# Performance work log

Hardware: AMD Instinct MI355X
Metric: run time of the kernel (lower is better)

The kernel has to match this reference:

```python
import jax, jax.numpy as jnp
import numpy as np

B, S, D, H, DFF = 4, 2048, 1024, 16, 4096
HD = D // H
EPS = 1e-12

def _layernorm(x, g, b):
    mu = jnp.mean(x, axis=-1, keepdims=True)
    var = jnp.mean(jnp.square(x - mu), axis=-1, keepdims=True)
    return (x - mu) * jax.lax.rsqrt(var + EPS) * g + b

def setup_inputs() -> dict:
    key = jax.random.key(0)
    ks = jax.random.split(key, 12)
    sd = 0.02
    inp = {
        'hidden_states': jax.random.normal(ks[0], (B, S, D), jnp.float32),
        'attention_mask': jnp.zeros((B, 1, 1, S), jnp.float32),
        'Wq': jax.random.normal(ks[1], (D, D), jnp.float32) * sd,
        'bq': jnp.zeros((D,), jnp.float32),
        'Wk': jax.random.normal(ks[2], (D, D), jnp.float32) * sd,
        'bk': jnp.zeros((D,), jnp.float32),
        'Wv': jax.random.normal(ks[3], (D, D), jnp.float32) * sd,
        'bv': jnp.zeros((D,), jnp.float32),
        'Wo': jax.random.normal(ks[4], (D, D), jnp.float32) * sd,
        'bo': jnp.zeros((D,), jnp.float32),
        'ln1_g': jnp.ones((D,), jnp.float32),
        'ln1_b': jnp.zeros((D,), jnp.float32),
        'Wi': jax.random.normal(ks[5], (D, DFF), jnp.float32) * sd,
        'bi': jnp.zeros((DFF,), jnp.float32),
        'Wo2': jax.random.normal(ks[6], (DFF, D), jnp.float32) * sd,
        'bo2': jnp.zeros((D,), jnp.float32),
        'ln2_g': jnp.ones((D,), jnp.float32),
        'ln2_b': jnp.zeros((D,), jnp.float32),
    }
    return inp

def reference(hidden_states, attention_mask, Wq, bq, Wk, bk, Wv, bv, Wo, bo,
              ln1_g, ln1_b, Wi, bi, Wo2, bo2, ln2_g, ln2_b):
    x = hidden_states  # [B,S,D]
    # project and split heads -> [B,H,S,hd]
    def heads(t):
        return t.reshape(B, S, H, HD).transpose(0, 2, 1, 3)
    q = heads(x @ Wq + bq)
    k = heads(x @ Wk + bk)
    v = heads(x @ Wv + bv)
    scores = jnp.einsum('bhqd,bhkd->bhqk', q, k) / np.float32(np.sqrt(HD))
    scores = scores + attention_mask  # additive mask broadcast [B,1,1,S]
    weights = jax.nn.softmax(scores, axis=-1)
    ctx = jnp.einsum('bhqk,bhkd->bhqd', weights, v)
    ctx = ctx.transpose(0, 2, 1, 3).reshape(B, S, D)
    attn_out = _layernorm(ctx @ Wo + bo + x, ln1_g, ln1_b)
    # FFN (gelu) with residual + LayerNorm
    h = jax.nn.gelu(attn_out @ Wi + bi, approximate=False)
    out = _layernorm(h @ Wo2 + bo2 + attn_out, ln2_g, ln2_b)
    return out
```

## Files before the change

### kernel.cpp

```cpp
#include <hip/hip_runtime.h>
#include <hip/hip_bf16.h>
#include <math.h>

#define B_   4
#define S_   2048
#define D_   1024
#define H_   16
#define HD_  64
#define DFF_ 4096
#define M_   (B_*S_)

typedef __bf16 bf16x8 __attribute__((ext_vector_type(8)));
typedef __bf16 bf16x4 __attribute__((ext_vector_type(4)));
typedef float  floatx4 __attribute__((ext_vector_type(4)));

__device__ __forceinline__ float  b2f(__bf16 v) { return (float)v; }
__device__ __forceinline__ __bf16 f2b(float v)  { return (__bf16)v; }

__device__ __forceinline__ void async_ld16(const void* g, void* l) {
    __builtin_amdgcn_global_load_lds(
        (const __attribute__((address_space(1))) unsigned int*)g,
        (__attribute__((address_space(3))) unsigned int*)l, 16, 0, 0);
}

__global__ void transpose_conv_kernel(const float* __restrict__ in,
                                      __bf16* __restrict__ out, int R, int C,
                                      float scale)
{
    __shared__ float t[32][33];
    int c0 = blockIdx.x * 32, r0 = blockIdx.y * 32;
    int tx = threadIdx.x, ty = threadIdx.y;
    for (int i = ty; i < 32; i += 8)
        t[i][tx] = in[(long)(r0 + i) * C + c0 + tx];
    __syncthreads();
    for (int i = ty; i < 32; i += 8)
        out[(long)(c0 + i) * R + r0 + tx] = f2b(t[tx][i] * scale);
}

__global__ void vt_transpose_kernel(const __bf16* __restrict__ qkv,
                                    __bf16* __restrict__ vtg)
{
    __shared__ __bf16 t[32][34];
    int b  = blockIdx.z;
    int h  = blockIdx.y >> 1;
    int d0 = (blockIdx.y & 1) * 32;
    int s0 = blockIdx.x * 32;
    int tx = threadIdx.x, ty = threadIdx.y;
    for (int i = ty; i < 32; i += 8)
        t[i][tx] = qkv[(long)(b * S_ + s0 + i) * 3072 + 2048 + h * 64 + d0 + tx];
    __syncthreads();
    for (int i = ty; i < 32; i += 8)
        vtg[((long)(b * H_ + h) * 64 + d0 + i) * S_ + s0 + tx] = t[tx][i];
}

__global__ void f2b_kernel(const float* __restrict__ in, __bf16* __restrict__ out,
                           long n)
{
    long i = ((long)blockIdx.x * 256 + threadIdx.x) * 8;
    if (i >= n) return;
    float4 a = *(const float4*)&in[i];
    float4 c = *(const float4*)&in[i + 4];
    union { __bf16 h[8]; uint4 u; } p;
    p.h[0] = f2b(a.x); p.h[1] = f2b(a.y); p.h[2] = f2b(a.z); p.h[3] = f2b(a.w);
    p.h[4] = f2b(c.x); p.h[5] = f2b(c.y); p.h[6] = f2b(c.z); p.h[7] = f2b(c.w);
    *(uint4*)&out[i] = p.u;
}

__global__ void bias_concat_kernel(const float* __restrict__ bq,
                                   const float* __restrict__ bk,
                                   const float* __restrict__ bv,
                                   float* __restrict__ dst)
{
    int i = blockIdx.x * 256 + threadIdx.x;
    if (i >= 3 * D_) return;
    float v = (i < D_) ? bq[i] * 0.125f
            : (i < 2 * D_) ? bk[i - D_] : bv[i - 2 * D_];
    dst[i] = v;
}

template<int MODE>
__global__ __launch_bounds__(256, 2)
void gemm_kernel(const __bf16* __restrict__ A, const __bf16* __restrict__ Bt,
                 const float* __restrict__ bias, const float* __restrict__ resid,
                 float* __restrict__ Cf, __bf16* __restrict__ Cb,
                 int M, int N, int K)
{
    __shared__ __bf16 sA[128 * 64];
    __shared__ __bf16 sB[128 * 64];

    const int tid  = threadIdx.x;
    const int lane = tid & 63;
    const int wave = tid >> 6;
    const int wm   = (wave >> 1) * 64;
    const int wn   = (wave & 1) * 64;
    const long bm  = (long)blockIdx.y * 128;
    const long bn  = (long)blockIdx.x * 128;

    floatx4 acc[4][4];
#pragma unroll
    for (int i = 0; i < 4; ++i)
#pragma unroll
        for (int j = 0; j < 4; ++j)
#pragma unroll
            for (int r = 0; r < 4; ++r) acc[i][j][r] = 0.0f;

    const int mrow = lane & 15;
    const int quad = lane >> 4;
    const int koff0 = ((0 * 4 + quad) ^ (mrow & 7)) * 8;
    const int koff1 = ((1 * 4 + quad) ^ (mrow & 7)) * 8;

    for (int k0 = 0; k0 < K; k0 += 64) {
        __syncthreads();
#pragma unroll
        for (int t = 0; t < 4; ++t) {
            int ci  = tid + t * 256;
            int row = ci >> 3;
            int col = ((ci & 7) ^ (row & 7)) << 3;
            async_ld16(A  + (bm + row) * (long)K + k0 + col, &sA[ci * 8]);
            async_ld16(Bt + (bn + row) * (long)K + k0 + col, &sB[ci * 8]);
        }
        __syncthreads();

#pragma unroll
        for (int s = 0; s < 2; ++s) {
            const int ko = s ? koff1 : koff0;
            bf16x8 a[4], b[4];
#pragma unroll
            for (int i = 0; i < 4; ++i)
                a[i] = *(const bf16x8*)&sA[(wm + i * 16 + mrow) * 64 + ko];
#pragma unroll
            for (int j = 0; j < 4; ++j)
                b[j] = *(const bf16x8*)&sB[(wn + j * 16 + mrow) * 64 + ko];
#pragma unroll
            for (int i = 0; i < 4; ++i)
#pragma unroll
                for (int j = 0; j < 4; ++j)
                    acc[i][j] = __builtin_amdgcn_mfma_f32_16x16x32_bf16(
                        a[i], b[j], acc[i][j], 0, 0, 0);
        }
    }

    const int rq = quad * 4;
    const int cn = lane & 15;
#pragma unroll
    for (int i = 0; i < 4; ++i) {
#pragma unroll
        for (int j = 0; j < 4; ++j) {
            long col = bn + wn + j * 16 + cn;
            float bv = bias[col];
#pragma unroll
            for (int r = 0; r < 4; ++r) {
                long row = bm + wm + i * 16 + rq + r;
                float v = acc[i][j][r] + bv;
                if (MODE == 0) {
                    Cb[row * N + col] = f2b(v);
                } else if (MODE == 1) {
                    Cf[row * N + col] = v + resid[row * N + col];
                } else {
                    float g = 0.5f * v * (1.0f + erff(v * 0.70710678118654752f));
                    Cb[row * N + col] = f2b(g);
                }
            }
        }
    }
}

__global__ __launch_bounds__(256, 2)
void attn_kernel(const __bf16* __restrict__ QKV, const __bf16* __restrict__ VT,
                 const float* __restrict__ mask, __bf16* __restrict__ ctx)
{
    __shared__ __bf16 Qs[64 * 64];
    __shared__ __bf16 Ks[64 * 64];
    __shared__ __bf16 Vt[64 * 64];
    __shared__ __bf16 Ps[64 * 64];

    const int tid  = threadIdx.x;
    const int lane = tid & 63;
    const int wave = tid >> 6;
    const int w16  = wave * 16;
    const int b    = blockIdx.z, h = blockIdx.y;
    const int q0   = blockIdx.x * 64;
    const int cn   = lane & 15;
    const int quad = lane >> 4;
    const int rq   = quad * 4;
    const int koff0 = ((0 * 4 + quad) ^ (cn & 7)) * 8;
    const int koff1 = ((1 * 4 + quad) ^ (cn & 7)) * 8;

#pragma unroll
    for (int t = 0; t < 2; ++t) {
        int ci = tid + t * 256;
        int qr = ci >> 3, dc = ((ci & 7) ^ (qr & 7)) << 3;
        async_ld16(QKV + (long)(b * S_ + q0 + qr) * 3072 + h * 64 + dc,
                   &Qs[ci * 8]);
    }
    __syncthreads();
    const bf16x8 aq0 = *(const bf16x8*)&Qs[(w16 + cn) * 64 + koff0];
    const bf16x8 aq1 = *(const bf16x8*)&Qs[(w16 + cn) * 64 + koff1];

    float l_[4];
    floatx4 o_[4];
#pragma unroll
    for (int r = 0; r < 4; ++r) l_[r] = 0.0f;
#pragma unroll
    for (int jt = 0; jt < 4; ++jt)
#pragma unroll
        for (int r = 0; r < 4; ++r) o_[jt][r] = 0.0f;

    const long vbase = ((long)(b * H_ + h) * 64) * S_;

    for (int k0 = 0; k0 < S_; k0 += 64) {
        __syncthreads();
#pragma unroll
        for (int t = 0; t < 2; ++t) {
            int ci = tid + t * 256;
            int kr = ci >> 3, dc = ((ci & 7) ^ (kr & 7)) << 3;
            async_ld16(QKV + (long)(b * S_ + k0 + kr) * 3072 + 1024 + h * 64 + dc,
                       &Ks[ci * 8]);
            int vd = ci >> 3, kc = ((ci & 7) ^ (vd & 7)) << 3;
            async_ld16(VT + vbase + (long)vd * S_ + k0 + kc, &Vt[ci * 8]);
        }
        __syncthreads();

        floatx4 st[4];
#pragma unroll
        for (int jt = 0; jt < 4; ++jt)
#pragma unroll
            for (int r = 0; r < 4; ++r) st[jt][r] = 0.0f;
#pragma unroll
        for (int jt = 0; jt < 4; ++jt) {
            bf16x8 b0 = *(const bf16x8*)&Ks[(jt * 16 + cn) * 64 + koff0];
            bf16x8 b1 = *(const bf16x8*)&Ks[(jt * 16 + cn) * 64 + koff1];
            st[jt] = __builtin_amdgcn_mfma_f32_16x16x32_bf16(aq0, b0, st[jt], 0, 0, 0);
            st[jt] = __builtin_amdgcn_mfma_f32_16x16x32_bf16(aq1, b1, st[jt], 0, 0, 0);
        }
#pragma unroll
        for (int jt = 0; jt < 4; ++jt) {
            float mv = mask[(long)b * S_ + k0 + jt * 16 + cn] - 8.0f;
#pragma unroll
            for (int r = 0; r < 4; ++r) {
                float p = __expf(st[jt][r] + mv);
                st[jt][r] = p;
                l_[r] += p;
            }
        }
#pragma unroll
        for (int jt = 0; jt < 4; ++jt)
#pragma unroll
            for (int r = 0; r < 4; ++r) {
                int prow = w16 + rq + r;
                int pcol = (((jt * 2 + (cn >> 3)) ^ (prow & 7)) << 3) + (cn & 7);
                Ps[prow * 64 + pcol] = f2b(st[jt][r]);
            }

        {
            bf16x8 ap0 = *(const bf16x8*)&Ps[(w16 + cn) * 64 + koff0];
            bf16x8 ap1 = *(const bf16x8*)&Ps[(w16 + cn) * 64 + koff1];
#pragma unroll
            for (int jt = 0; jt < 4; ++jt) {
                bf16x8 b0 = *(const bf16x8*)&Vt[(jt * 16 + cn) * 64 + koff0];
                bf16x8 b1 = *(const bf16x8*)&Vt[(jt * 16 + cn) * 64 + koff1];
                o_[jt] = __builtin_amdgcn_mfma_f32_16x16x32_bf16(ap0, b0, o_[jt], 0, 0, 0);
                o_[jt] = __builtin_amdgcn_mfma_f32_16x16x32_bf16(ap1, b1, o_[jt], 0, 0, 0);
            }
        }
    }

#pragma unroll
    for (int r = 0; r < 4; ++r) {
        float l = l_[r];
        l += __shfl_xor(l, 1);
        l += __shfl_xor(l, 2);
        l += __shfl_xor(l, 4);
        l += __shfl_xor(l, 8);
        float linv = 1.0f / l;
        long rowg = (long)(b * S_ + q0 + w16 + rq + r) * D_ + h * 64;
#pragma unroll
        for (int jt = 0; jt < 4; ++jt)
            ctx[rowg + jt * 16 + cn] = f2b(o_[jt][r] * linv);
    }
}

__global__ __launch_bounds__(256)
void ln_kernel(const float* __restrict__ X, const float* __restrict__ gamma,
               const float* __restrict__ beta, float* __restrict__ out,
               __bf16* __restrict__ outb)
{
    const long row = blockIdx.x;
    const int tid = threadIdx.x;
    const float* x = X + row * D_;
    float4 v = *(const float4*)&x[tid * 4];
    float s  = v.x + v.y + v.z + v.w;
    float s2 = v.x * v.x + v.y * v.y + v.z * v.z + v.w * v.w;
    for (int off = 32; off > 0; off >>= 1) {
        s  += __shfl_down(s, off);
        s2 += __shfl_down(s2, off);
    }
    __shared__ float red[8];
    int wave = tid >> 6, lane = tid & 63;
    if (lane == 0) { red[wave] = s; red[4 + wave] = s2; }
    __syncthreads();
    float ts  = red[0] + red[1] + red[2] + red[3];
    float ts2 = red[4] + red[5] + red[6] + red[7];
    float mu  = ts * (1.0f / D_);
    float var = ts2 * (1.0f / D_) - mu * mu;
    float rs  = rsqrtf(fmaxf(var, 0.0f) + 1e-12f);
    float4 g = *(const float4*)&gamma[tid * 4];
    float4 b = *(const float4*)&beta[tid * 4];
    float4 o;
    o.x = (v.x - mu) * rs * g.x + b.x;
    o.y = (v.y - mu) * rs * g.y + b.y;
    o.z = (v.z - mu) * rs * g.z + b.z;
    o.w = (v.w - mu) * rs * g.w + b.w;
    *(float4*)&out[row * D_ + tid * 4] = o;
    if (outb) {
        bf16x4 ob;
        ob[0] = f2b(o.x); ob[1] = f2b(o.y); ob[2] = f2b(o.z); ob[3] = f2b(o.w);
        *(bf16x4*)&outb[row * D_ + tid * 4] = ob;
    }
}

extern "C" void kernel_launch(void* const* d_in, const int* in_sizes, int n_in,
                              void* d_out, int out_size, void* d_ws, size_t ws_size,
                              hipStream_t stream)
{
    const float* hid  = (const float*)d_in[0];
    const float* mask = (const float*)d_in[1];
    const float* Wq   = (const float*)d_in[2];
    const float* bq   = (const float*)d_in[3];
    const float* Wk   = (const float*)d_in[4];
    const float* bk   = (const float*)d_in[5];
    const float* Wv   = (const float*)d_in[6];
    const float* bv   = (const float*)d_in[7];
    const float* Wo   = (const float*)d_in[8];
    const float* bo   = (const float*)d_in[9];
    const float* g1   = (const float*)d_in[10];
    const float* b1   = (const float*)d_in[11];
    const float* Wi   = (const float*)d_in[12];
    const float* bi   = (const float*)d_in[13];
    const float* Wo2  = (const float*)d_in[14];
    const float* bo2  = (const float*)d_in[15];
    const float* g2   = (const float*)d_in[16];
    const float* b2   = (const float*)d_in[17];
    float* out = (float*)d_out;

    char* w = (char*)d_ws;
    auto take = [&](size_t bytes) { char* p = w; w += bytes; return p; };
    __bf16* wqkvb = (__bf16*)take((size_t)3 * D_ * D_ * 2);
    __bf16* wob   = (__bf16*)take((size_t)D_ * D_ * 2);
    __bf16* wib   = (__bf16*)take((size_t)D_ * DFF_ * 2);
    __bf16* wo2b  = (__bf16*)take((size_t)D_ * DFF_ * 2);
    float*  qkvbias = (float*)take(16384);
    __bf16* qkv   = (__bf16*)take((size_t)M_ * 3 * D_ * 2);
    __bf16* ctxb  = (__bf16*)take((size_t)M_ * D_ * 2);
    __bf16* hb    = (__bf16*)take((size_t)M_ * D_ * 2);
    float*  tmp      = (float*)take((size_t)M_ * D_ * 4);
    float*  attn_out = (float*)take((size_t)M_ * D_ * 4);
    __bf16* hbuf = qkv;
    __bf16* vtg  = hb;
    __bf16* attn_out_b = hb;
    (void)in_sizes; (void)n_in; (void)out_size; (void)ws_size;

    dim3 tb(32, 8);
    transpose_conv_kernel<<<dim3(D_/32, D_/32), tb, 0, stream>>>(Wq, wqkvb,            D_, D_, 0.125f);
    transpose_conv_kernel<<<dim3(D_/32, D_/32), tb, 0, stream>>>(Wk, wqkvb + D_*D_,    D_, D_, 1.0f);
    transpose_conv_kernel<<<dim3(D_/32, D_/32), tb, 0, stream>>>(Wv, wqkvb + 2*D_*D_,  D_, D_, 1.0f);
    transpose_conv_kernel<<<dim3(D_/32, D_/32), tb, 0, stream>>>(Wo, wob, D_, D_, 1.0f);
    transpose_conv_kernel<<<dim3(DFF_/32, D_/32), tb, 0, stream>>>(Wi, wib, D_, DFF_, 1.0f);
    transpose_conv_kernel<<<dim3(D_/32, DFF_/32), tb, 0, stream>>>(Wo2, wo2b, DFF_, D_, 1.0f);
    bias_concat_kernel<<<12, 256, 0, stream>>>(bq, bk, bv, qkvbias);
    f2b_kernel<<<(M_*D_/8 + 255)/256, 256, 0, stream>>>(hid, hb, (long)M_*D_);

    gemm_kernel<0><<<dim3(3*D_/128, M_/128), 256, 0, stream>>>(
        hb, wqkvb, qkvbias, nullptr, nullptr, qkv, M_, 3*D_, D_);

    vt_transpose_kernel<<<dim3(S_/32, H_*2, B_), tb, 0, stream>>>(qkv, vtg);

    attn_kernel<<<dim3(S_/64, H_, B_), 256, 0, stream>>>(qkv, vtg, mask, ctxb);

    gemm_kernel<1><<<dim3(D_/128, M_/128), 256, 0, stream>>>(
        ctxb, wob, bo, hid, tmp, nullptr, M_, D_, D_);
    ln_kernel<<<M_, 256, 0, stream>>>(tmp, g1, b1, attn_out, attn_out_b);

    gemm_kernel<2><<<dim3(DFF_/128, M_/128), 256, 0, stream>>>(
        attn_out_b, wib, bi, nullptr, nullptr, hbuf, M_, DFF_, D_);
    gemm_kernel<1><<<dim3(D_/128, M_/128), 256, 0, stream>>>(
        hbuf, wo2b, bo2, attn_out, tmp, nullptr, M_, D_, DFF_);
    ln_kernel<<<M_, 256, 0, stream>>>(tmp, g2, b2, out, nullptr);
}
```

Baseline: 581.5 us.

## Switch attention to 32x32x16 MFMA with 128-query tiles per block

The attention kernel now processes 128 query rows per block (32 per wave) and uses 32x32x16 bf16 MFMA instructions instead of 16x16x32. Each K/V tile loaded into shared memory is reused across twice as many queries, halving K/V global traffic and the number of blocks. The row-sum reduction gains an extra shuffle step and register pressure per wave rises (two 16-wide accumulators plus 16 row sums), which may lower occupancy.

```diff
diff --git a/kernel.cpp b/kernel.cpp
--- a/kernel.cpp
+++ b/kernel.cpp
@@ -13,6 +13,7 @@
 typedef __bf16 bf16x8 __attribute__((ext_vector_type(8)));
 typedef __bf16 bf16x4 __attribute__((ext_vector_type(4)));
 typedef float  floatx4 __attribute__((ext_vector_type(4)));
+typedef float  floatx16 __attribute__((ext_vector_type(16)));
 
 __device__ __forceinline__ float  b2f(__bf16 v) { return (float)v; }
 __device__ __forceinline__ __bf16 f2b(float v)  { return (__bf16)v; }
@@ -169,42 +170,42 @@
 void attn_kernel(const __bf16* __restrict__ QKV, const __bf16* __restrict__ VT,
                  const float* __restrict__ mask, __bf16* __restrict__ ctx)
 {
-    __shared__ __bf16 Qs[64 * 64];
+    __shared__ __bf16 Qs[128 * 64];
     __shared__ __bf16 Ks[64 * 64];
     __shared__ __bf16 Vt[64 * 64];
-    __shared__ __bf16 Ps[64 * 64];
+    __shared__ __bf16 Ps[128 * 64];
 
     const int tid  = threadIdx.x;
     const int lane = tid & 63;
     const int wave = tid >> 6;
-    const int w16  = wave * 16;
+    const int w32  = wave * 32;
     const int b    = blockIdx.z, h = blockIdx.y;
-    const int q0   = blockIdx.x * 64;
-    const int cn   = lane & 15;
-    const int quad = lane >> 4;
-    const int rq   = quad * 4;
-    const int koff0 = ((0 * 4 + quad) ^ (cn & 7)) * 8;
-    const int koff1 = ((1 * 4 + quad) ^ (cn & 7)) * 8;
-
-#pragma unroll
-    for (int t = 0; t < 2; ++t) {
+    const int q0   = blockIdx.x * 128;
+    const int l31  = lane & 31;
+    const int half = lane >> 5;
+
+    int koff[4];
+#pragma unroll
+    for (int s = 0; s < 4; ++s)
+        koff[s] = ((s * 2 + half) ^ (l31 & 7)) * 8;
+
+#pragma unroll
+    for (int t = 0; t < 4; ++t) {
         int ci = tid + t * 256;
         int qr = ci >> 3, dc = ((ci & 7) ^ (qr & 7)) << 3;
         async_ld16(QKV + (long)(b * S_ + q0 + qr) * 3072 + h * 64 + dc,
                    &Qs[ci * 8]);
     }
     __syncthreads();
-    const bf16x8 aq0 = *(const bf16x8*)&Qs[(w16 + cn) * 64 + koff0];
-    const bf16x8 aq1 = *(const bf16x8*)&Qs[(w16 + cn) * 64 + koff1];
-
-    float l_[4];
-    floatx4 o_[4];
-#pragma unroll
-    for (int r = 0; r < 4; ++r) l_[r] = 0.0f;
-#pragma unroll
-    for (int jt = 0; jt < 4; ++jt)
-#pragma unroll
-        for (int r = 0; r < 4; ++r) o_[jt][r] = 0.0f;
+    bf16x8 aq[4];
+#pragma unroll
+    for (int s = 0; s < 4; ++s)
+        aq[s] = *(const bf16x8*)&Qs[(w32 + l31) * 64 + koff[s]];
+
+    float l_[16];
+    floatx16 o_[2];
+#pragma unroll
+    for (int r = 0; r < 16; ++r) { l_[r] = 0.0f; o_[0][r] = 0.0f; o_[1][r] = 0.0f; }
 
     const long vbase = ((long)(b * H_ + h) * 64) * S_;
 
@@ -216,67 +217,65 @@
             int kr = ci >> 3, dc = ((ci & 7) ^ (kr & 7)) << 3;
             async_ld16(QKV + (long)(b * S_ + k0 + kr) * 3072 + 1024 + h * 64 + dc,
                        &Ks[ci * 8]);
-            int vd = ci >> 3, kc = ((ci & 7) ^ (vd & 7)) << 3;
-            async_ld16(VT + vbase + (long)vd * S_ + k0 + kc, &Vt[ci * 8]);
+            async_ld16(VT + vbase + (long)kr * S_ + k0 + dc, &Vt[ci * 8]);
         }
         __syncthreads();
 
-        floatx4 st[4];
-#pragma unroll
-        for (int jt = 0; jt < 4; ++jt)
-#pragma unroll
-            for (int r = 0; r < 4; ++r) st[jt][r] = 0.0f;
-#pragma unroll
-        for (int jt = 0; jt < 4; ++jt) {
-            bf16x8 b0 = *(const bf16x8*)&Ks[(jt * 16 + cn) * 64 + koff0];
-            bf16x8 b1 = *(const bf16x8*)&Ks[(jt * 16 + cn) * 64 + koff1];
-            st[jt] = __builtin_amdgcn_mfma_f32_16x16x32_bf16(aq0, b0, st[jt], 0, 0, 0);
-            st[jt] = __builtin_amdgcn_mfma_f32_16x16x32_bf16(aq1, b1, st[jt], 0, 0, 0);
-        }
-#pragma unroll
-        for (int jt = 0; jt < 4; ++jt) {
-            float mv = mask[(long)b * S_ + k0 + jt * 16 + cn] - 8.0f;
-#pragma unroll
-            for (int r = 0; r < 4; ++r) {
-                float p = __expf(st[jt][r] + mv);
-                st[jt][r] = p;
+        floatx16 st[2];
+#pragma unroll
+        for (int r = 0; r < 16; ++r) { st[0][r] = 0.0f; st[1][r] = 0.0f; }
+#pragma unroll
+        for (int nt = 0; nt < 2; ++nt) {
+#pragma unroll
+            for (int s = 0; s < 4; ++s) {
+                bf16x8 bk = *(const bf16x8*)&Ks[(nt * 32 + l31) * 64 + koff[s]];
+                st[nt] = __builtin_amdgcn_mfma_f32_32x32x16_bf16(aq[s], bk, st[nt], 0, 0, 0);
+            }
+        }
+#pragma unroll
+        for (int nt = 0; nt < 2; ++nt) {
+            float mv = mask[(long)b * S_ + k0 + nt * 32 + l31] - 8.0f;
+#pragma unroll
+            for (int r = 0; r < 16; ++r) {
+                float p = __expf(st[nt][r] + mv);
+                st[nt][r] = p;
                 l_[r] += p;
             }
         }
 #pragma unroll
-        for (int jt = 0; jt < 4; ++jt)
-#pragma unroll
-            for (int r = 0; r < 4; ++r) {
-                int prow = w16 + rq + r;
-                int pcol = (((jt * 2 + (cn >> 3)) ^ (prow & 7)) << 3) + (cn & 7);
-                Ps[prow * 64 + pcol] = f2b(st[jt][r]);
-            }
-
-        {
-            bf16x8 ap0 = *(const bf16x8*)&Ps[(w16 + cn) * 64 + koff0];
-            bf16x8 ap1 = *(const bf16x8*)&Ps[(w16 + cn) * 64 + koff1];
-#pragma unroll
-            for (int jt = 0; jt < 4; ++jt) {
-                bf16x8 b0 = *(const bf16x8*)&Vt[(jt * 16 + cn) * 64 + koff0];
-                bf16x8 b1 = *(const bf16x8*)&Vt[(jt * 16 + cn) * 64 + koff1];
-                o_[jt] = __builtin_amdgcn_mfma_f32_16x16x32_bf16(ap0, b0, o_[jt], 0, 0, 0);
-                o_[jt] = __builtin_amdgcn_mfma_f32_16x16x32_bf16(ap1, b1, o_[jt], 0, 0, 0);
-            }
-        }
-    }
-
-#pragma unroll
-    for (int r = 0; r < 4; ++r) {
+        for (int nt = 0; nt < 2; ++nt)
+#pragma unroll
+            for (int r = 0; r < 16; ++r) {
+                int prow = w32 + (r & 3) + 8 * (r >> 2) + 4 * half;
+                int col  = nt * 32 + l31;
+                int sc   = (((col >> 3) ^ (prow & 7)) << 3) | (col & 7);
+                Ps[prow * 64 + sc] = f2b(st[nt][r]);
+            }
+
+#pragma unroll
+        for (int s = 0; s < 4; ++s) {
+            bf16x8 ap = *(const bf16x8*)&Ps[(w32 + l31) * 64 + koff[s]];
+#pragma unroll
+            for (int nt = 0; nt < 2; ++nt) {
+                bf16x8 bv = *(const bf16x8*)&Vt[(nt * 32 + l31) * 64 + koff[s]];
+                o_[nt] = __builtin_amdgcn_mfma_f32_32x32x16_bf16(ap, bv, o_[nt], 0, 0, 0);
+            }
+        }
+    }
+
+#pragma unroll
+    for (int r = 0; r < 16; ++r) {
         float l = l_[r];
         l += __shfl_xor(l, 1);
         l += __shfl_xor(l, 2);
         l += __shfl_xor(l, 4);
         l += __shfl_xor(l, 8);
+        l += __shfl_xor(l, 16);
         float linv = 1.0f / l;
-        long rowg = (long)(b * S_ + q0 + w16 + rq + r) * D_ + h * 64;
-#pragma unroll
-        for (int jt = 0; jt < 4; ++jt)
-            ctx[rowg + jt * 16 + cn] = f2b(o_[jt][r] * linv);
+        int row = w32 + (r & 3) + 8 * (r >> 2) + 4 * half;
+        long rowg = (long)(b * S_ + q0 + row) * D_ + h * 64;
+        ctx[rowg + l31]      = f2b(o_[0][r] * linv);
+        ctx[rowg + 32 + l31] = f2b(o_[1][r] * linv);
     }
 }
 
@@ -375,7 +374,7 @@
 
     vt_transpose_kernel<<<dim3(S_/32, H_*2, B_), tb, 0, stream>>>(qkv, vtg);
 
-    attn_kernel<<<dim3(S_/64, H_, B_), 256, 0, stream>>>(qkv, vtg, mask, ctxb);
+    attn_kernel<<<dim3(S_/128, H_, B_), 256, 0, stream>>>(qkv, vtg, mask, ctxb);
 
     gemm_kernel<1><<<dim3(D_/128, M_/128), 256, 0, stream>>>(
         ctxb, wob, bo, hid, tmp, nullptr, M_, D_, D_);
```

After: 622.9 us. 1.07x slower.

## Double attention query tile per block and fold log2e into Q scaling

Applied to the files above, without the earlier changes.

The attention kernel now handles 128 query rows per block, 32 per wave, so each K and V tile loaded into shared memory feeds twice as many MFMAs. This halves the K/V traffic per query. The Q and P buffers are merged to hold shared-memory use roughly constant. The softmax scale now includes log2(e) through the Q weights and bias so the kernel can call exp2f instead of __expf. The trade-off is more accumulator registers per thread and half as many blocks, which lowers parallelism.

```diff
diff --git a/kernel.cpp b/kernel.cpp
--- a/kernel.cpp
+++ b/kernel.cpp
@@ -69,11 +69,11 @@
 __global__ void bias_concat_kernel(const float* __restrict__ bq,
                                    const float* __restrict__ bk,
                                    const float* __restrict__ bv,
-                                   float* __restrict__ dst)
+                                   float* __restrict__ dst, float qscale)
 {
     int i = blockIdx.x * 256 + threadIdx.x;
     if (i >= 3 * D_) return;
-    float v = (i < D_) ? bq[i] * 0.125f
+    float v = (i < D_) ? bq[i] * qscale
             : (i < 2 * D_) ? bk[i - D_] : bv[i - 2 * D_];
     dst[i] = v;
 }
@@ -169,17 +169,16 @@
 void attn_kernel(const __bf16* __restrict__ QKV, const __bf16* __restrict__ VT,
                  const float* __restrict__ mask, __bf16* __restrict__ ctx)
 {
-    __shared__ __bf16 Qs[64 * 64];
+    __shared__ __bf16 QPs[128 * 64];
     __shared__ __bf16 Ks[64 * 64];
     __shared__ __bf16 Vt[64 * 64];
-    __shared__ __bf16 Ps[64 * 64];
 
     const int tid  = threadIdx.x;
     const int lane = tid & 63;
     const int wave = tid >> 6;
-    const int w16  = wave * 16;
+    const int w32  = wave * 32;
     const int b    = blockIdx.z, h = blockIdx.y;
-    const int q0   = blockIdx.x * 64;
+    const int q0   = blockIdx.x * 128;
     const int cn   = lane & 15;
     const int quad = lane >> 4;
     const int rq   = quad * 4;
@@ -187,26 +186,33 @@
     const int koff1 = ((1 * 4 + quad) ^ (cn & 7)) * 8;
 
 #pragma unroll
-    for (int t = 0; t < 2; ++t) {
+    for (int t = 0; t < 4; ++t) {
         int ci = tid + t * 256;
         int qr = ci >> 3, dc = ((ci & 7) ^ (qr & 7)) << 3;
         async_ld16(QKV + (long)(b * S_ + q0 + qr) * 3072 + h * 64 + dc,
-                   &Qs[ci * 8]);
+                   &QPs[ci * 8]);
     }
     __syncthreads();
-    const bf16x8 aq0 = *(const bf16x8*)&Qs[(w16 + cn) * 64 + koff0];
-    const bf16x8 aq1 = *(const bf16x8*)&Qs[(w16 + cn) * 64 + koff1];
-
-    float l_[4];
-    floatx4 o_[4];
-#pragma unroll
-    for (int r = 0; r < 4; ++r) l_[r] = 0.0f;
-#pragma unroll
-    for (int jt = 0; jt < 4; ++jt)
-#pragma unroll
-        for (int r = 0; r < 4; ++r) o_[jt][r] = 0.0f;
+    bf16x8 aq[2][2];
+#pragma unroll
+    for (int g = 0; g < 2; ++g) {
+        aq[g][0] = *(const bf16x8*)&QPs[(w32 + g * 16 + cn) * 64 + koff0];
+        aq[g][1] = *(const bf16x8*)&QPs[(w32 + g * 16 + cn) * 64 + koff1];
+    }
+
+    float l_[2][4];
+    floatx4 o_[2][4];
+#pragma unroll
+    for (int g = 0; g < 2; ++g)
+#pragma unroll
+        for (int r = 0; r < 4; ++r) {
+            l_[g][r] = 0.0f;
+#pragma unroll
+            for (int jt = 0; jt < 4; ++jt) o_[g][jt][r] = 0.0f;
+        }
 
     const long vbase = ((long)(b * H_ + h) * 64) * S_;
+    const float LOG2E = 1.44269504088896f;
 
     for (int k0 = 0; k0 < S_; k0 += 64) {
         __syncthreads();
@@ -216,68 +222,79 @@
             int kr = ci >> 3, dc = ((ci & 7) ^ (kr & 7)) << 3;
             async_ld16(QKV + (long)(b * S_ + k0 + kr) * 3072 + 1024 + h * 64 + dc,
                        &Ks[ci * 8]);
-            int vd = ci >> 3, kc = ((ci & 7) ^ (vd & 7)) << 3;
-            async_ld16(VT + vbase + (long)vd * S_ + k0 + kc, &Vt[ci * 8]);
+            async_ld16(VT + vbase + (long)kr * S_ + k0 + dc, &Vt[ci * 8]);
         }
         __syncthreads();
 
-        floatx4 st[4];
-#pragma unroll
-        for (int jt = 0; jt < 4; ++jt)
-#pragma unroll
-            for (int r = 0; r < 4; ++r) st[jt][r] = 0.0f;
+        floatx4 st[2][4];
+#pragma unroll
+        for (int g = 0; g < 2; ++g)
+#pragma unroll
+            for (int jt = 0; jt < 4; ++jt)
+#pragma unroll
+                for (int r = 0; r < 4; ++r) st[g][jt][r] = 0.0f;
+#pragma unroll
+        for (int s = 0; s < 2; ++s) {
+            const int ko = s ? koff1 : koff0;
+#pragma unroll
+            for (int jt = 0; jt < 4; ++jt) {
+                bf16x8 bk = *(const bf16x8*)&Ks[(jt * 16 + cn) * 64 + ko];
+                st[0][jt] = __builtin_amdgcn_mfma_f32_16x16x32_bf16(aq[0][s], bk, st[0][jt], 0, 0, 0);
+                st[1][jt] = __builtin_amdgcn_mfma_f32_16x16x32_bf16(aq[1][s], bk, st[1][jt], 0, 0, 0);
+            }
+        }
 #pragma unroll
         for (int jt = 0; jt < 4; ++jt) {
-            bf16x8 b0 = *(const bf16x8*)&Ks[(jt * 16 + cn) * 64 + koff0];
-            bf16x8 b1 = *(const bf16x8*)&Ks[(jt * 16 + cn) * 64 + koff1];
-            st[jt] = __builtin_amdgcn_mfma_f32_16x16x32_bf16(aq0, b0, st[jt], 0, 0, 0);
-            st[jt] = __builtin_amdgcn_mfma_f32_16x16x32_bf16(aq1, b1, st[jt], 0, 0, 0);
-        }
-#pragma unroll
-        for (int jt = 0; jt < 4; ++jt) {
-            float mv = mask[(long)b * S_ + k0 + jt * 16 + cn] - 8.0f;
-#pragma unroll
-            for (int r = 0; r < 4; ++r) {
-                float p = __expf(st[jt][r] + mv);
-                st[jt][r] = p;
-                l_[r] += p;
+            float mv = (mask[(long)b * S_ + k0 + jt * 16 + cn] - 8.0f) * LOG2E;
+#pragma unroll
+            for (int g = 0; g < 2; ++g)
+#pragma unroll
+                for (int r = 0; r < 4; ++r) {
+                    float p = exp2f(st[g][jt][r] + mv);
+                    st[g][jt][r] = p;
+                    l_[g][r] += p;
+                }
+        }
+#pragma unroll
+        for (int g = 0; g < 2; ++g)
+#pragma unroll
+            for (int jt = 0; jt < 4; ++jt)
+#pragma unroll
+                for (int r = 0; r < 4; ++r) {
+                    int prow = w32 + g * 16 + rq + r;
+                    int pcol = (((jt * 2 + (cn >> 3)) ^ (prow & 7)) << 3) + (cn & 7);
+                    QPs[prow * 64 + pcol] = f2b(st[g][jt][r]);
+                }
+
+#pragma unroll
+        for (int s = 0; s < 2; ++s) {
+            const int ko = s ? koff1 : koff0;
+            bf16x8 ap0 = *(const bf16x8*)&QPs[(w32 + cn) * 64 + ko];
+            bf16x8 ap1 = *(const bf16x8*)&QPs[(w32 + 16 + cn) * 64 + ko];
+#pragma unroll
+            for (int jt = 0; jt < 4; ++jt) {
+                bf16x8 bv = *(const bf16x8*)&Vt[(jt * 16 + cn) * 64 + ko];
+                o_[0][jt] = __builtin_amdgcn_mfma_f32_16x16x32_bf16(ap0, bv, o_[0][jt], 0, 0, 0);
+                o_[1][jt] = __builtin_amdgcn_mfma_f32_16x16x32_bf16(ap1, bv, o_[1][jt], 0, 0, 0);
             }
         }
-#pragma unroll
-        for (int jt = 0; jt < 4; ++jt)
-#pragma unroll
-            for (int r = 0; r < 4; ++r) {
-                int prow = w16 + rq + r;
-                int pcol = (((jt * 2 + (cn >> 3)) ^ (prow & 7)) << 3) + (cn & 7);
-                Ps[prow * 64 + pcol] = f2b(st[jt][r]);
-            }
-
-        {
-            bf16x8 ap0 = *(const bf16x8*)&Ps[(w16 + cn) * 64 + koff0];
-            bf16x8 ap1 = *(const bf16x8*)&Ps[(w16 + cn) * 64 + koff1];
-#pragma unroll
-            for (int jt = 0; jt < 4; ++jt) {
-                bf16x8 b0 = *(const bf16x8*)&Vt[(jt * 16 + cn) * 64 + koff0];
-                bf16x8 b1 = *(const bf16x8*)&Vt[(jt * 16 + cn) * 64 + koff1];
-                o_[jt] = __builtin_amdgcn_mfma_f32_16x16x32_bf16(ap0, b0, o_[jt], 0, 0, 0);
-                o_[jt] = __builtin_amdgcn_mfma_f32_16x16x32_bf16(ap1, b1, o_[jt], 0, 0, 0);
-            }
-        }
-    }
-
-#pragma unroll
-    for (int r = 0; r < 4; ++r) {
-        float l = l_[r];
-        l += __shfl_xor(l, 1);
-        l += __shfl_xor(l, 2);
-        l += __shfl_xor(l, 4);
-        l += __shfl_xor(l, 8);
-        float linv = 1.0f / l;
-        long rowg = (long)(b * S_ + q0 + w16 + rq + r) * D_ + h * 64;
-#pragma unroll
-        for (int jt = 0; jt < 4; ++jt)
-            ctx[rowg + jt * 16 + cn] = f2b(o_[jt][r] * linv);
-    }
+    }
+
+#pragma unroll
+    for (int g = 0; g < 2; ++g)
+#pragma unroll
+        for (int r = 0; r < 4; ++r) {
+            float l = l_[g][r];
+            l += __shfl_xor(l, 1);
+            l += __shfl_xor(l, 2);
+            l += __shfl_xor(l, 4);
+            l += __shfl_xor(l, 8);
+            float linv = 1.0f / l;
+            long rowg = (long)(b * S_ + q0 + w32 + g * 16 + rq + r) * D_ + h * 64;
+#pragma unroll
+            for (int jt = 0; jt < 4; ++jt)
+                ctx[rowg + jt * 16 + cn] = f2b(o_[g][jt][r] * linv);
+        }
 }
 
 __global__ __launch_bounds__(256)
@@ -360,14 +377,16 @@
     __bf16* attn_out_b = hb;
     (void)in_sizes; (void)n_in; (void)out_size; (void)ws_size;
 
+    const float QSC = 0.125f * 1.44269504088896f;
+
     dim3 tb(32, 8);
-    transpose_conv_kernel<<<dim3(D_/32, D_/32), tb, 0, stream>>>(Wq, wqkvb,            D_, D_, 0.125f);
+    transpose_conv_kernel<<<dim3(D_/32, D_/32), tb, 0, stream>>>(Wq, wqkvb,            D_, D_, QSC);
     transpose_conv_kernel<<<dim3(D_/32, D_/32), tb, 0, stream>>>(Wk, wqkvb + D_*D_,    D_, D_, 1.0f);
     transpose_conv_kernel<<<dim3(D_/32, D_/32), tb, 0, stream>>>(Wv, wqkvb + 2*D_*D_,  D_, D_, 1.0f);
     transpose_conv_kernel<<<dim3(D_/32, D_/32), tb, 0, stream>>>(Wo, wob, D_, D_, 1.0f);
     transpose_conv_kernel<<<dim3(DFF_/32, D_/32), tb, 0, stream>>>(Wi, wib, D_, DFF_, 1.0f);
     transpose_conv_kernel<<<dim3(D_/32, DFF_/32), tb, 0, stream>>>(Wo2, wo2b, DFF_, D_, 1.0f);
-    bias_concat_kernel<<<12, 256, 0, stream>>>(bq, bk, bv, qkvbias);
+    bias_concat_kernel<<<12, 256, 0, stream>>>(bq, bk, bv, qkvbias, QSC);
     f2b_kernel<<<(M_*D_/8 + 255)/256, 256, 0, stream>>>(hid, hb, (long)M_*D_);
 
     gemm_kernel<0><<<dim3(3*D_/128, M_/128), 256, 0, stream>>>(
@@ -375,7 +394,7 @@
 
     vt_transpose_kernel<<<dim3(S_/32, H_*2, B_), tb, 0, stream>>>(qkv, vtg);
 
-    attn_kernel<<<dim3(S_/64, H_, B_), 256, 0, stream>>>(qkv, vtg, mask, ctxb);
+    attn_kernel<<<dim3(S_/128, H_, B_), 256, 0, stream>>>(qkv, vtg, mask, ctxb);
 
     gemm_kernel<1><<<dim3(D_/128, M_/128), 256, 0, stream>>>(
         ctxb, wob, bo, hid, tmp, nullptr, M_, D_, D_);
```

Measured after the change: 606.9 us. +4.4%, slower.
